# Kernel tuning notes

Measured on AMD Instinct MI355X. Metric: run time of the kernel, lower is better.

Reference implementation:

```python
import jax, jax.numpy as jnp
import numpy as np

B, L, DIM, HID, DSSH, DSSN = 2, 4096, 1024, 4096, 512, 512


def _ln(x, w, b):
    # LayerNorm over last dim, eps=1e-5 (torch default)
    m = x.mean(-1, keepdims=True)
    v = ((x - m) ** 2).mean(-1, keepdims=True)
    return (x - m) * jax.lax.rsqrt(v + 1e-5) * w + b


def _dss(x, n2_w, n2_b, LR, LI, CR, CI, D):
    # x: [B, L, dss_hidden]
    Lseq = x.shape[-2]
    xn = _ln(x, n2_w, n2_b)
    Lam = (-jnp.exp(LR) + 1j * jnp.exp(LI)).astype(jnp.complex64)        # [N]
    t = jnp.arange(Lseq, dtype=jnp.float32)
    S = jnp.exp(Lam[:, None] * t[None, :])                               # [N, L]
    Cc = (CR + 1j * CI) * ((jnp.exp(Lam) - 1.0) / Lam)                   # [H, N]
    K = jnp.einsum('hn,nl->lh', Cc, S).real                              # [L, H]
    n2 = 2 * Lseq
    Kf = jnp.fft.rfft(K, n=n2, axis=-2)                                  # [L+1, H]
    uf = jnp.fft.rfft(xn, n=n2, axis=-2)                                 # [B, L+1, H]
    y = jnp.fft.irfft(uf * Kf, n=n2, axis=-2)[..., :Lseq, :]
    return y + D * xn


def setup_inputs() -> dict:
    key = jax.random.key(0)
    ks = jax.random.split(key, 12)
    s = lambda k, sh, sc=1.0: jax.random.normal(k, sh, jnp.float32) * sc
    return dict(
        idx=s(ks[0], (B, L, DIM)),
        n1_w=jnp.ones((DIM,), jnp.float32), n1_b=jnp.zeros((DIM,), jnp.float32),
        Wxg=s(ks[1], (DIM, HID), 0.02),
        Wdin=s(ks[2], (DIM, DSSH), 0.02),
        n2_w=jnp.ones((DSSH,), jnp.float32), n2_b=jnp.zeros((DSSH,), jnp.float32),
        LR=s(ks[3], (DSSN,)), LI=s(ks[4], (DSSN,)),
        CR=s(ks[5], (DSSH, DSSN), 0.1), CI=s(ks[6], (DSSH, DSSN), 0.1),
        D=s(ks[7], (DSSH,)),
        Wgate=s(ks[8], (DSSH, HID), 0.02),
        Wout=s(ks[9], (HID, DIM), 0.02), bout=jnp.zeros((DIM,), jnp.float32),
    )


def reference(idx, n1_w, n1_b, Wxg, Wdin, n2_w, n2_b, LR, LI, CR, CI, D, Wgate, Wout, bout):
    x = _ln(idx, n1_w, n1_b)
    xg = x @ Wxg                                            # [B, L, HID]
    d = _dss(x @ Wdin, n2_w, n2_b, LR, LI, CR, CI, D)       # [B, L, DSSH]
    g = d @ Wgate                                           # [B, L, HID]
    out = (g * xg) @ Wout + bout                            # dropout is identity in eval
    return out + idx
```

## Files before the change

kernel.cpp:

```cpp
#include <hip/hip_runtime.h>
#include <math.h>


typedef unsigned short u16;
typedef unsigned int u32;
typedef __attribute__((ext_vector_type(8))) __bf16 bf16x8;
typedef __attribute__((ext_vector_type(4))) float f32x4;
typedef __attribute__((ext_vector_type(4))) u32 u32x4;

__device__ __forceinline__ u16 f2bf(float f) {
  u32 u = __float_as_uint(f);
  u32 r = u + 0x7FFFu + ((u >> 16) & 1u);
  return (u16)(r >> 16);
}
__device__ __forceinline__ float bf2f(u16 h) { return __uint_as_float(((u32)h) << 16); }

__global__ __launch_bounds__(256) void trans_conv(
    const float* __restrict__ in, u16* __restrict__ out, int K, int N) {
  __shared__ float t[32][33];
  int tx = threadIdx.x & 31, ty = threadIdx.x >> 5;
  int nb = N >> 5;
  int k0 = (blockIdx.x / nb) << 5;
  int n0 = (blockIdx.x % nb) << 5;
#pragma unroll
  for (int i = 0; i < 32; i += 8)
    t[ty + i][tx] = in[(size_t)(k0 + ty + i) * N + n0 + tx];
  __syncthreads();
#pragma unroll
  for (int i = 0; i < 32; i += 8)
    out[(size_t)(n0 + ty + i) * K + k0 + tx] = f2bf(t[tx][ty + i]);
}

__global__ __launch_bounds__(256) void trans_bf(
    const u16* __restrict__ in, u16* __restrict__ out, int R, int C) {
  __shared__ u16 t[32][34];
  int tx = threadIdx.x & 31, ty = threadIdx.x >> 5;
  int nb = C >> 5;
  int r0 = (blockIdx.x / nb) << 5;
  int c0 = (blockIdx.x % nb) << 5;
#pragma unroll
  for (int i = 0; i < 32; i += 8)
    t[ty + i][tx] = in[(size_t)(r0 + ty + i) * C + c0 + tx];
  __syncthreads();
#pragma unroll
  for (int i = 0; i < 32; i += 8)
    out[(size_t)(c0 + ty + i) * R + r0 + tx] = t[tx][ty + i];
}

template <bool BOUT>
__global__ void ln_kernel(const float* __restrict__ in, const float* __restrict__ gw,
                          const float* __restrict__ gb, void* outp, int D) {
  int row = blockIdx.x;
  int tid = threadIdx.x;
  const float4* r4 = (const float4*)(in + (size_t)row * D);
  float4 v = r4[tid];
  float s = v.x + v.y + v.z + v.w;
  float ss = fmaf(v.x, v.x, fmaf(v.y, v.y, fmaf(v.z, v.z, v.w * v.w)));
#pragma unroll
  for (int o = 32; o >= 1; o >>= 1) { s += __shfl_xor(s, o); ss += __shfl_xor(ss, o); }
  __shared__ float sa[8], sb[8];
  int nw = blockDim.x >> 6;
  if ((tid & 63) == 0) { sa[tid >> 6] = s; sb[tid >> 6] = ss; }
  __syncthreads();
  float S = 0.f, SS = 0.f;
  for (int i = 0; i < nw; ++i) { S += sa[i]; SS += sb[i]; }
  float mean = S / (float)D;
  float var = SS / (float)D - mean * mean;
  float inv = rsqrtf(var + 1e-5f);
  float4 wv = ((const float4*)gw)[tid];
  float4 bv = ((const float4*)gb)[tid];
  float o0 = (v.x - mean) * inv * wv.x + bv.x;
  float o1 = (v.y - mean) * inv * wv.y + bv.y;
  float o2 = (v.z - mean) * inv * wv.z + bv.z;
  float o3 = (v.w - mean) * inv * wv.w + bv.w;
  if (BOUT) {
    ushort4 o; o.x = f2bf(o0); o.y = f2bf(o1); o.z = f2bf(o2); o.w = f2bf(o3);
    ((ushort4*)outp)[(size_t)row * (D >> 2) + tid] = o;
  } else {
    float4 o; o.x = o0; o.y = o1; o.z = o2; o.w = o3;
    ((float4*)outp)[(size_t)row * (D >> 2) + tid] = o;
  }
}

__global__ __launch_bounds__(256) void ln_stats(
    const u16* __restrict__ xdTb, float* __restrict__ meanv, float* __restrict__ invv) {
  int lane = threadIdx.x & 63;
  int seg = threadIdx.x >> 6;
  int col = blockIdx.x * 64 + lane;
  float s = 0.f, ss = 0.f;
  const u16* p = xdTb + (size_t)(seg * 128) * 8192 + col;
#pragma unroll 8
  for (int r = 0; r < 128; ++r) {
    float v = bf2f(p[(size_t)r * 8192]);
    s += v; ss = fmaf(v, v, ss);
  }
  __shared__ float sa[4][64], sb[4][64];
  sa[seg][lane] = s; sb[seg][lane] = ss;
  __syncthreads();
  if (threadIdx.x < 64) {
    float S = sa[0][lane] + sa[1][lane] + sa[2][lane] + sa[3][lane];
    float SS = sb[0][lane] + sb[1][lane] + sb[2][lane] + sb[3][lane];
    float mean = S * (1.0f / 512.0f);
    float var = SS * (1.0f / 512.0f) - mean * mean;
    meanv[blockIdx.x * 64 + lane] = mean;
    invv[blockIdx.x * 64 + lane] = rsqrtf(var + 1e-5f);
  }
}

template <int MODE>
__global__ __launch_bounds__(256, 2) void gemm128p(
    const u16* __restrict__ A, const u16* __restrict__ Bt,
    int M, int N, int K,
    float* Cf, u16* Cb, const u16* aux,
    const float* __restrict__ bias, const float* __restrict__ res) {
  constexpr int BUF = 16384;
  __shared__ __align__(16) u16 lds[2 * BUF];
  const int tid = threadIdx.x;
  const int lane = tid & 63;
  const int w = tid >> 6;
  const int nwg = (int)gridDim.x;
  const int cpx = nwg >> 3;
  const int bid = (nwg & 7) ? (int)blockIdx.x
                            : ((int)blockIdx.x & 7) * cpx + ((int)blockIdx.x >> 3);
  const int tiles_n = N >> 7;
  const int tm = (bid / tiles_n) << 7;
  const int tn = (bid % tiles_n) << 7;

  const int wm = w >> 1, wn = w & 1;
  const int lr = lane & 15;
  const int kq = lane >> 4;
  const int l7 = lane & 7;
  const int rsub = lane >> 3;
  const int sslot = (lane & 7) ^ rsub;
  const u16* gA = A + (size_t)(tm + w * 32 + rsub) * K + sslot * 8;
  const u16* gB = Bt + (size_t)(tn + w * 32 + rsub) * K + sslot * 8;
  auto ldsc = (__attribute__((address_space(3))) char*)lds;

  auto STAGE = [&](int kt, int c) {
    const size_t kof = (size_t)kt << 6;
#pragma unroll
    for (int i = 0; i < 4; ++i) {
      u32 da = (u32)(c * BUF + (w * 32 + i * 8) * 64) * 2u;
      __builtin_amdgcn_global_load_lds(
          (const __attribute__((address_space(1))) void*)(gA + (size_t)(i * 8) * K + kof),
          (__attribute__((address_space(3))) void*)(ldsc + da), 16, 0, 0);
      __builtin_amdgcn_global_load_lds(
          (const __attribute__((address_space(1))) void*)(gB + (size_t)(i * 8) * K + kof),
          (__attribute__((address_space(3))) void*)(ldsc + da + 16384), 16, 0, 0);
    }
  };

  f32x4 acc[4][4] = {};
  const int NT = K >> 6;

  STAGE(0, 0);
  asm volatile("s_waitcnt vmcnt(0)" ::: "memory");
  __builtin_amdgcn_s_barrier();
  __builtin_amdgcn_sched_barrier(0);

  int cur = 0;
  for (int kt = 0; kt < NT; ++kt) {
    if (kt + 1 < NT) STAGE(kt + 1, cur ^ 1);
    const u32 ab = (u32)cur * BUF;
#pragma unroll
    for (int ks = 0; ks < 2; ++ks) {
      const int slp = ((((ks << 2) | kq)) ^ l7) << 3;
      bf16x8 af[4], bv[4];
#pragma unroll
      for (int mi = 0; mi < 4; ++mi) {
        int ra = wm * 64 + mi * 16 + lr;
        af[mi] = *(const bf16x8*)&lds[ab + ra * 64 + slp];
      }
#pragma unroll
      for (int ni = 0; ni < 4; ++ni) {
        int rb = wn * 64 + ni * 16 + lr;
        bv[ni] = *(const bf16x8*)&lds[ab + 8192 + rb * 64 + slp];
      }
      __builtin_amdgcn_s_setprio(1);
#pragma unroll
      for (int mi = 0; mi < 4; ++mi)
#pragma unroll
        for (int ni = 0; ni < 4; ++ni)
          acc[mi][ni] = __builtin_amdgcn_mfma_f32_16x16x32_bf16(af[mi], bv[ni], acc[mi][ni], 0, 0, 0);
      __builtin_amdgcn_s_setprio(0);
    }
    asm volatile("s_waitcnt vmcnt(0)" ::: "memory");
    __builtin_amdgcn_s_barrier();
    __builtin_amdgcn_sched_barrier(0);
    cur ^= 1;
  }

  float* lf = (float*)lds + w * (16 * 68);
  const int er = lane >> 2;
  const int ec = (lane & 3) << 4;
  const int gcol = tn + wn * 64 + ec;
#pragma unroll
  for (int mi = 0; mi < 4; ++mi) {
#pragma unroll
    for (int ni = 0; ni < 4; ++ni)
#pragma unroll
      for (int j = 0; j < 4; ++j)
        lf[(kq * 4 + j) * 68 + ni * 16 + lr] = acc[mi][ni][j];
    float v[16];
#pragma unroll
    for (int q = 0; q < 4; ++q)
      *(f32x4*)&v[q * 4] = *(const f32x4*)&lf[er * 68 + ec + q * 4];
    const int gr = tm + wm * 64 + mi * 16 + er;
    if (MODE == 3) {
      const float* rr = res + (size_t)gr * N + gcol;
      const float* br = bias + gcol;
      float* orr = Cf + (size_t)gr * N + gcol;
#pragma unroll
      for (int q = 0; q < 4; ++q) {
        f32x4 rv = *(const f32x4*)(rr + q * 4);
        f32x4 bv4 = *(const f32x4*)(br + q * 4);
        f32x4 ov;
        ov[0] = v[q * 4 + 0] + bv4[0] + rv[0];
        ov[1] = v[q * 4 + 1] + bv4[1] + rv[1];
        ov[2] = v[q * 4 + 2] + bv4[2] + rv[2];
        ov[3] = v[q * 4 + 3] + bv4[3] + rv[3];
        *(f32x4*)(orr + q * 4) = ov;
      }
    } else {
      u32 pk[8];
      if (MODE == 2) {
        const u16* ar = aux + (size_t)gr * N + gcol;
        u32x4 a0 = *(const u32x4*)ar;
        u32x4 a1 = *(const u32x4*)(ar + 8);
        u32 aw[8] = {a0[0], a0[1], a0[2], a0[3], a1[0], a1[1], a1[2], a1[3]};
#pragma unroll
        for (int e = 0; e < 8; ++e) {
          float m0 = v[2 * e] * bf2f((u16)(aw[e] & 0xffffu));
          float m1 = v[2 * e + 1] * bf2f((u16)(aw[e] >> 16));
          pk[e] = (u32)f2bf(m0) | ((u32)f2bf(m1) << 16);
        }
      } else {
#pragma unroll
        for (int e = 0; e < 8; ++e)
          pk[e] = (u32)f2bf(v[2 * e]) | ((u32)f2bf(v[2 * e + 1]) << 16);
      }
      u16* orr = Cb + (size_t)gr * N + gcol;
      *(u32x4*)orr = u32x4{pk[0], pk[1], pk[2], pk[3]};
      *(u32x4*)(orr + 8) = u32x4{pk[4], pk[5], pk[6], pk[7]};
    }
  }
}

__global__ __launch_bounds__(256) void kgen_s(
    const float* __restrict__ LR, const float* __restrict__ LI, u16* __restrict__ SRSI) {
  int idx0 = blockIdx.x * 256 + threadIdx.x;
  int l = idx0 >> 10;
  int kk = idx0 & 1023;
  int n = kk & 511;
  double a = exp((double)LR[n]);
  double om = exp((double)LI[n]);
  double ld = (double)l;
  float decay = (float)exp(-a * ld);
  double th = fmod(om * ld, 6.283185307179586477);
  float c, s;
  sincosf((float)th, &s, &c);
  SRSI[idx0] = f2bf(decay * ((kk < 512) ? c : s));
}

__global__ __launch_bounds__(256) void kgen_c(
    const float* __restrict__ LR, const float* __restrict__ LI,
    const float* __restrict__ CR, const float* __restrict__ CI, u16* __restrict__ Ct) {
  int idx0 = blockIdx.x * 256 + threadIdx.x;
  int h = idx0 >> 9, n = idx0 & 511;
  float eLR = expf(LR[n]), eLI = expf(LI[n]);
  float lre = -eLR, lim = eLI;
  float er = expf(lre);
  float c, s;
  sincosf(lim, &s, &c);
  float wr = er * c - 1.0f, wi = er * s;
  float den = lre * lre + lim * lim;
  float gr = (wr * lre + wi * lim) / den;
  float gi = (wi * lre - wr * lim) / den;
  float cr = CR[(size_t)h * 512 + n], ci = CI[(size_t)h * 512 + n];
  float ccr = cr * gr - ci * gi;
  float cci = cr * gi + ci * gr;
  Ct[(size_t)h * 1024 + n] = f2bf(ccr);
  Ct[(size_t)h * 1024 + 512 + n] = f2bf(-cci);
}

__global__ __launch_bounds__(256) void twfill(float4* __restrict__ twg4) {
  int j = blockIdx.x * 256 + threadIdx.x;
  float t1 = -6.2831853071795864769f * (float)j / 8192.0f;
  float s1, c1, s2, c2;
  sincosf(t1, &s1, &c1);
  sincosf(2.0f * t1, &s2, &c2);
  twg4[j] = {c1, s1, c2, s2};
}

struct C2 { float x, y; };
__device__ __forceinline__ C2 cadd(C2 a, C2 b) { return {a.x + b.x, a.y + b.y}; }
__device__ __forceinline__ C2 csub(C2 a, C2 b) { return {a.x - b.x, a.y - b.y}; }
__device__ __forceinline__ C2 cmul(C2 a, C2 b) {
  return {a.x * b.x - a.y * b.y, a.x * b.y + a.y * b.x};
}
__device__ __forceinline__ C2 cmulni(C2 a) { return {a.y, -a.x}; }

__device__ __forceinline__ int swz(int a) {
  return a ^ ((a >> 7) & 15) ^ ((a >> 11) & 3) ^ ((a >> 2) & 8) ^ ((a >> 3) & 2) ^ ((a >> 4) & 4);
}

#define BR13(x) ((int)(__brev((u32)(x)) >> 19))
#define RS 0.70710678118654752f

__device__ __forceinline__ void dif4(C2& a, C2& b, C2& c, C2& d, float4 wv) {
  C2 w = {wv.x, wv.y}, wm = {wv.y, -wv.x}, w2 = {wv.z, wv.w};
  C2 a1 = cadd(a, c);
  C2 c1 = cmul(csub(a, c), w);
  C2 b1 = cadd(b, d);
  C2 d1 = cmul(csub(b, d), wm);
  a = cadd(a1, b1);
  b = cmul(csub(a1, b1), w2);
  c = cadd(c1, d1);
  d = cmul(csub(c1, d1), w2);
}
__device__ __forceinline__ void dit4(C2& a, C2& b, C2& c, C2& d, float4 wv) {
  C2 w = {wv.x, wv.y}, wm = {wv.y, -wv.x}, wa = {wv.z, wv.w};
  C2 t = cmul(wa, b);
  C2 a1 = cadd(a, t), b1 = csub(a, t);
  C2 u = cmul(wa, d);
  C2 c1 = cadd(c, u), d1 = csub(c, u);
  C2 v = cmul(w, c1);
  C2 xx = cmul(wm, d1);
  a = cadd(a1, v);
  c = csub(a1, v);
  b = cadd(b1, xx);
  d = csub(b1, xx);
}

template <int L>
__device__ __forceinline__ void dif16(C2* z, int tid, const float4* __restrict__ twg4) {
  const int Q = 1 << (L - 2);
  const int pos2 = tid & (Q - 1);
  const int i0 = ((tid >> (L - 2)) << (L + 2)) | pos2;
  int ad[16]; C2 x[16];
#pragma unroll
  for (int k = 0; k < 16; ++k) { ad[k] = swz(i0 + k * Q); x[k] = z[ad[k]]; }
#pragma unroll
  for (int r = 0; r < 4; ++r)
    dif4(x[r], x[r + 4], x[r + 8], x[r + 12], twg4[(pos2 + r * Q) << (11 - L)]);
  {
    float4 wv2 = twg4[pos2 << (13 - L)];
#pragma unroll
    for (int m = 0; m < 4; ++m)
      dif4(x[4 * m], x[4 * m + 1], x[4 * m + 2], x[4 * m + 3], wv2);
  }
#pragma unroll
  for (int k = 0; k < 16; ++k) z[ad[k]] = x[k];
}
template <int L>
__device__ __forceinline__ void dit16(C2* z, int tid, const float4* __restrict__ twg4) {
  const int Q = 1 << (L - 2);
  const int pos2 = tid & (Q - 1);
  const int i0 = ((tid >> (L - 2)) << (L + 2)) | pos2;
  int ad[16]; C2 x[16];
#pragma unroll
  for (int k = 0; k < 16; ++k) { ad[k] = swz(i0 + k * Q); x[k] = z[ad[k]]; }
  {
    float4 wv2 = twg4[pos2 << (13 - L)];
#pragma unroll
    for (int m = 0; m < 4; ++m)
      dit4(x[4 * m], x[4 * m + 1], x[4 * m + 2], x[4 * m + 3], wv2);
  }
#pragma unroll
  for (int r = 0; r < 4; ++r)
    dit4(x[r], x[r + 4], x[r + 8], x[r + 12], twg4[(pos2 + r * Q) << (11 - L)]);
#pragma unroll
  for (int k = 0; k < 16; ++k) z[ad[k]] = x[k];
}

template <int LOGM>
__device__ __forceinline__ void dif_pass(C2* z, int tid, const float4* __restrict__ twg4) {
  const int M4 = 1 << LOGM;
#pragma unroll
  for (int j = 0; j < 4; ++j) {
    int b = tid + j * 512;
    int pos = b & (M4 - 1);
    int i0 = ((b >> LOGM) << (LOGM + 2)) | pos;
    int ia = swz(i0), ib = swz(i0 + M4), ic = swz(i0 + 2 * M4), id = swz(i0 + 3 * M4);
    C2 a = z[ia], bb = z[ib], c = z[ic], d = z[id];
    float4 wv = twg4[pos << (11 - LOGM)];
    dif4(a, bb, c, d, wv);
    z[ia] = a; z[ib] = bb; z[ic] = c; z[id] = d;
  }
}

template <int LOGM>
__device__ __forceinline__ void dit_pass(C2* z, int tid, const float4* __restrict__ twg4) {
  const int M4 = 1 << LOGM;
#pragma unroll
  for (int j = 0; j < 4; ++j) {
    int b = tid + j * 512;
    int pos = b & (M4 - 1);
    int i0 = ((b >> LOGM) << (LOGM + 2)) | pos;
    int ia = swz(i0), ib = swz(i0 + M4), ic = swz(i0 + 2 * M4), id = swz(i0 + 3 * M4);
    C2 a = z[ia], bb = z[ib], c = z[ic], d = z[id];
    float4 wv = twg4[pos << (11 - LOGM)];
    dit4(a, bb, c, d, wv);
    z[ia] = a; z[ib] = bb; z[ic] = c; z[id] = d;
  }
}

__device__ __forceinline__ void dif_r8(C2* z, int tid) {
#pragma unroll
  for (int j = 0; j < 2; ++j) {
    int base = (tid + j * 512) << 3;
    int ad[8]; C2 x[8];
#pragma unroll
    for (int e = 0; e < 8; ++e) { ad[e] = swz(base + e); x[e] = z[ad[e]]; }
    C2 t;
    t = csub(x[0], x[4]); x[0] = cadd(x[0], x[4]); x[4] = t;
    t = csub(x[1], x[5]); x[1] = cadd(x[1], x[5]); x[5] = cmul(t, {RS, -RS});
    t = csub(x[2], x[6]); x[2] = cadd(x[2], x[6]); x[6] = cmulni(t);
    t = csub(x[3], x[7]); x[3] = cadd(x[3], x[7]); x[7] = cmul(t, {-RS, -RS});
    t = csub(x[0], x[2]); x[0] = cadd(x[0], x[2]); x[2] = t;
    t = csub(x[1], x[3]); x[1] = cadd(x[1], x[3]); x[3] = cmulni(t);
    t = csub(x[4], x[6]); x[4] = cadd(x[4], x[6]); x[6] = t;
    t = csub(x[5], x[7]); x[5] = cadd(x[5], x[7]); x[7] = cmulni(t);
    t = csub(x[0], x[1]); x[0] = cadd(x[0], x[1]); x[1] = t;
    t = csub(x[2], x[3]); x[2] = cadd(x[2], x[3]); x[3] = t;
    t = csub(x[4], x[5]); x[4] = cadd(x[4], x[5]); x[5] = t;
    t = csub(x[6], x[7]); x[6] = cadd(x[6], x[7]); x[7] = t;
#pragma unroll
    for (int e = 0; e < 8; ++e) z[ad[e]] = x[e];
  }
}

__device__ __forceinline__ void r8_fused(C2* z, int tid, const u32* __restrict__ kfr) {
#pragma unroll
  for (int j = 0; j < 2; ++j) {
    int base = (tid + j * 512) << 3;
    int ad[8]; C2 x[8];
#pragma unroll
    for (int e = 0; e < 8; ++e) { ad[e] = swz(base + e); x[e] = z[ad[e]]; }
    u32x4 k0 = *(const u32x4*)(kfr + base);
    u32x4 k1 = *(const u32x4*)(kfr + base + 4);
    u32 kw[8] = {k0[0], k0[1], k0[2], k0[3], k1[0], k1[1], k1[2], k1[3]};
    C2 t;
    t = csub(x[0], x[4]); x[0] = cadd(x[0], x[4]); x[4] = t;
    t = csub(x[1], x[5]); x[1] = cadd(x[1], x[5]); x[5] = cmul(t, {RS, -RS});
    t = csub(x[2], x[6]); x[2] = cadd(x[2], x[6]); x[6] = cmulni(t);
    t = csub(x[3], x[7]); x[3] = cadd(x[3], x[7]); x[7] = cmul(t, {-RS, -RS});
    t = csub(x[0], x[2]); x[0] = cadd(x[0], x[2]); x[2] = t;
    t = csub(x[1], x[3]); x[1] = cadd(x[1], x[3]); x[3] = cmulni(t);
    t = csub(x[4], x[6]); x[4] = cadd(x[4], x[6]); x[6] = t;
    t = csub(x[5], x[7]); x[5] = cadd(x[5], x[7]); x[7] = cmulni(t);
    t = csub(x[0], x[1]); x[0] = cadd(x[0], x[1]); x[1] = t;
    t = csub(x[2], x[3]); x[2] = cadd(x[2], x[3]); x[3] = t;
    t = csub(x[4], x[5]); x[4] = cadd(x[4], x[5]); x[5] = t;
    t = csub(x[6], x[7]); x[6] = cadd(x[6], x[7]); x[7] = t;
#pragma unroll
    for (int e = 0; e < 8; ++e) {
      C2 kf = {bf2f((u16)(kw[e] & 0xffffu)), bf2f((u16)(kw[e] >> 16))};
      C2 pr = cmul(x[e], kf);
      x[e] = {pr.x, -pr.y};
    }
    t = x[1]; x[1] = csub(x[0], t); x[0] = cadd(x[0], t);
    t = x[3]; x[3] = csub(x[2], t); x[2] = cadd(x[2], t);
    t = x[5]; x[5] = csub(x[4], t); x[4] = cadd(x[4], t);
    t = x[7]; x[7] = csub(x[6], t); x[6] = cadd(x[6], t);
    t = x[2];          x[2] = csub(x[0], t); x[0] = cadd(x[0], t);
    t = cmulni(x[3]);  x[3] = csub(x[1], t); x[1] = cadd(x[1], t);
    t = x[6];          x[6] = csub(x[4], t); x[4] = cadd(x[4], t);
    t = cmulni(x[7]);  x[7] = csub(x[5], t); x[5] = cadd(x[5], t);
    t = x[4];                    x[4] = csub(x[0], t); x[0] = cadd(x[0], t);
    t = cmul(x[5], {RS, -RS});   x[5] = csub(x[1], t); x[1] = cadd(x[1], t);
    t = cmulni(x[6]);            x[6] = csub(x[2], t); x[2] = cadd(x[2], t);
    t = cmul(x[7], {-RS, -RS});  x[7] = csub(x[3], t); x[3] = cadd(x[3], t);
#pragma unroll
    for (int e = 0; e < 8; ++e) z[ad[e]] = x[e];
  }
}

__global__ __launch_bounds__(512) void kfft2(
    const u16* __restrict__ KTb, const float4* __restrict__ twg4,
    u32* __restrict__ Kfb) {
  __shared__ C2 z[8192];
  const int g = blockIdx.x;
  const int t = threadIdx.x;
  const u16* k0r = KTb + ((size_t)(2 * g) << 12);
  const u16* k1r = KTb + ((size_t)(2 * g + 1) << 12);

  C2 x[16];
#pragma unroll
  for (int k = 0; k < 8; ++k) {
    int l = t + k * 512;
    x[k] = {bf2f(k0r[l]), bf2f(k1r[l])};
  }
#pragma unroll
  for (int k = 8; k < 16; ++k) x[k] = {0.f, 0.f};
#pragma unroll
  for (int r = 0; r < 4; ++r)
    dif4(x[r], x[r + 4], x[r + 8], x[r + 12], twg4[t + r * 512]);
  {
    float4 wv2 = twg4[t << 2];
#pragma unroll
    for (int m = 0; m < 4; ++m)
      dif4(x[4 * m], x[4 * m + 1], x[4 * m + 2], x[4 * m + 3], wv2);
  }
#pragma unroll
  for (int k = 0; k < 16; ++k) z[swz(t + k * 512)] = x[k];
  __syncthreads();

  dif16<7>(z, t, twg4);   __syncthreads();
  dif_pass<3>(z, t, twg4); __syncthreads();
  dif_r8(z, t);            __syncthreads();

  u32* o0 = Kfb + ((size_t)(2 * g) << 13);
  u32* o1 = Kfb + ((size_t)(2 * g + 1) << 13);
#pragma unroll
  for (int it = 0; it < 16; ++it) {
    int p = t + it * 512;
    int k = BR13(p);
    int km = (8192 - k) & 8191;
    int p2 = BR13(km);
    C2 Zk = z[swz(p)], Zm = z[swz(p2)];
    float f0r = 0.5f * (Zk.x + Zm.x), f0i = 0.5f * (Zk.y - Zm.y);
    float f1r = 0.5f * (Zk.y + Zm.y), f1i = 0.5f * (Zm.x - Zk.x);
    o0[p] = (u32)f2bf(f0r) | ((u32)f2bf(f0i) << 16);
    o1[p] = (u32)f2bf(f1r) | ((u32)f2bf(f1i) << 16);
  }
}

__global__ __launch_bounds__(512) void fft_conv4(
    const u16* __restrict__ xdTb, const u32* __restrict__ Kfb,
    const float* __restrict__ meanv, const float* __restrict__ invv,
    const float* __restrict__ n2w, const float* __restrict__ n2b,
    const float* __restrict__ Dv, const float4* __restrict__ twg4,
    u16* __restrict__ dT) {
  __shared__ C2 z[8192];
  const int h = blockIdx.x;
  const int t = threadIdx.x;
  const u16* xr = xdTb + ((size_t)h << 13);
  const float w2h = n2w[h], b2h = n2b[h], Dh = Dv[h];

  float xn0r[8], xn1r[8];
  C2 x[16];
#pragma unroll
  for (int k = 0; k < 8; ++k) {
    int l = t + k * 512;
    float x0 = bf2f(xr[l]);
    float x1 = bf2f(xr[4096 + l]);
    xn0r[k] = (x0 - meanv[l]) * invv[l] * w2h + b2h;
    xn1r[k] = (x1 - meanv[4096 + l]) * invv[4096 + l] * w2h + b2h;
    x[k] = {xn0r[k], xn1r[k]};
  }
#pragma unroll
  for (int k = 8; k < 16; ++k) x[k] = {0.f, 0.f};
#pragma unroll
  for (int r = 0; r < 4; ++r)
    dif4(x[r], x[r + 4], x[r + 8], x[r + 12], twg4[t + r * 512]);
  {
    float4 wv2 = twg4[t << 2];
#pragma unroll
    for (int m = 0; m < 4; ++m)
      dif4(x[4 * m], x[4 * m + 1], x[4 * m + 2], x[4 * m + 3], wv2);
  }
#pragma unroll
  for (int k = 0; k < 16; ++k) z[swz(t + k * 512)] = x[k];
  __syncthreads();

  dif16<7>(z, t, twg4);    __syncthreads();
  dif_pass<3>(z, t, twg4);  __syncthreads();
  r8_fused(z, t, Kfb + ((size_t)h << 13)); __syncthreads();
  dit_pass<3>(z, t, twg4);  __syncthreads();
  dit16<7>(z, t, twg4);     __syncthreads();

#pragma unroll
  for (int k = 0; k < 16; ++k) x[k] = z[swz(t + k * 512)];
  {
    float4 wv2 = twg4[t << 2];
#pragma unroll
    for (int m = 0; m < 4; ++m)
      dit4(x[4 * m], x[4 * m + 1], x[4 * m + 2], x[4 * m + 3], wv2);
  }
  const float sc = 1.0f / 8192.0f;
  u16* drow = dT + ((size_t)h << 13);
#pragma unroll
  for (int r = 0; r < 4; ++r) {
    float4 wv = twg4[t + r * 512];
    C2 w = {wv.x, wv.y}, wm = {wv.y, -wv.x}, wa = {wv.z, wv.w};
    C2 a = x[r], bb = x[r + 4], c = x[r + 8], d = x[r + 12];
    C2 tt = cmul(wa, bb);
    C2 a1 = cadd(a, tt), b1 = csub(a, tt);
    C2 u = cmul(wa, d);
    C2 c1 = cadd(c, u), d1 = csub(c, u);
    C2 olo = cadd(a1, cmul(w, c1));
    C2 ohi = cadd(b1, cmul(wm, d1));
    int l0 = t + r * 512;
    int l1 = t + (r + 4) * 512;
    drow[l0] = f2bf(fmaf(Dh, xn0r[r], olo.x * sc));
    drow[4096 + l0] = f2bf(fmaf(Dh, xn1r[r], -olo.y * sc));
    drow[l1] = f2bf(fmaf(Dh, xn0r[r + 4], ohi.x * sc));
    drow[4096 + l1] = f2bf(fmaf(Dh, xn1r[r + 4], -ohi.y * sc));
  }
}

extern "C" void kernel_launch(void* const* d_in, const int* in_sizes, int n_in,
                              void* d_out, int out_size, void* d_ws, size_t ws_size,
                              hipStream_t stream) {
  (void)in_sizes; (void)n_in; (void)out_size; (void)ws_size;
  const float* idx  = (const float*)d_in[0];
  const float* n1w  = (const float*)d_in[1];
  const float* n1b  = (const float*)d_in[2];
  const float* Wxg  = (const float*)d_in[3];
  const float* Wdin = (const float*)d_in[4];
  const float* n2w  = (const float*)d_in[5];
  const float* n2b  = (const float*)d_in[6];
  const float* LR   = (const float*)d_in[7];
  const float* LI   = (const float*)d_in[8];
  const float* CR   = (const float*)d_in[9];
  const float* CI   = (const float*)d_in[10];
  const float* Dv   = (const float*)d_in[11];
  const float* Wgate= (const float*)d_in[12];
  const float* Wout = (const float*)d_in[13];
  const float* bout = (const float*)d_in[14];
  float* out = (float*)d_out;

  const int Bn = 2, L = 4096, DIM = 1024, HID = 4096, H = 512;
  const int M = Bn * L;

  char* p = (char*)d_ws;
  auto alloc = [&](size_t bytes) { char* q = p; p += (bytes + 255) & ~(size_t)255; return q; };
  u16* Wxg_t   = (u16*)alloc((size_t)HID * DIM * 2);
  u16* Wdin_t  = (u16*)alloc((size_t)H * DIM * 2);
  u16* Wgate_t = (u16*)alloc((size_t)HID * H * 2);
  u16* Wout_t  = (u16*)alloc((size_t)DIM * HID * 2);
  u16* xbf     = (u16*)alloc((size_t)M * DIM * 2);
  u16* xg      = (u16*)alloc((size_t)M * HID * 2);
  u16* xdTb    = (u16*)alloc((size_t)H * M * 2);
  float* meanv = (float*)alloc((size_t)M * 4);
  float* invv  = (float*)alloc((size_t)M * 4);
  u16* SRSI    = (u16*)alloc((size_t)L * 1024 * 2);
  u16* Ct      = (u16*)alloc((size_t)H * 1024 * 2);
  u16* KTb     = (u16*)alloc((size_t)H * L * 2);
  u16* dTm     = (u16*)alloc((size_t)H * M * 2);
  u16* dbuf    = (u16*)alloc((size_t)M * H * 2);
  float4* twg4 = (float4*)alloc((size_t)2048 * 16);
  u32* Kfb = (u32*)xbf;

  trans_conv<<<dim3((DIM / 32) * (HID / 32)), 256, 0, stream>>>(Wxg, Wxg_t, DIM, HID);
  trans_conv<<<dim3((DIM / 32) * (H / 32)), 256, 0, stream>>>(Wdin, Wdin_t, DIM, H);
  trans_conv<<<dim3((H / 32) * (HID / 32)), 256, 0, stream>>>(Wgate, Wgate_t, H, HID);
  trans_conv<<<dim3((HID / 32) * (DIM / 32)), 256, 0, stream>>>(Wout, Wout_t, HID, DIM);
  twfill<<<dim3(8), 256, 0, stream>>>(twg4);
  ln_kernel<true><<<dim3(M), 256, 0, stream>>>(idx, n1w, n1b, xbf, DIM);
  gemm128p<1><<<dim3((M / 128) * (HID / 128)), 256, 0, stream>>>(
      xbf, Wxg_t, M, HID, DIM, nullptr, xg, nullptr, nullptr, nullptr);
  gemm128p<1><<<dim3((H / 128) * (M / 128)), 256, 0, stream>>>(
      Wdin_t, xbf, H, M, DIM, nullptr, xdTb, nullptr, nullptr, nullptr);
  ln_stats<<<dim3(M / 64), 256, 0, stream>>>(xdTb, meanv, invv);
  kgen_s<<<dim3(L * 1024 / 256), 256, 0, stream>>>(LR, LI, SRSI);
  kgen_c<<<dim3(H * 512 / 256), 256, 0, stream>>>(LR, LI, CR, CI, Ct);
  gemm128p<1><<<dim3((H / 128) * (L / 128)), 256, 0, stream>>>(
      Ct, SRSI, H, L, 1024, nullptr, KTb, nullptr, nullptr, nullptr);
  kfft2<<<dim3(H / 2), 512, 0, stream>>>(KTb, twg4, Kfb);
  fft_conv4<<<dim3(H), 512, 0, stream>>>(xdTb, Kfb, meanv, invv, n2w, n2b, Dv, twg4, dTm);
  trans_bf<<<dim3((H / 32) * (M / 32)), 256, 0, stream>>>(dTm, dbuf, H, M);
  gemm128p<2><<<dim3((M / 128) * (HID / 128)), 256, 0, stream>>>(
      dbuf, Wgate_t, M, HID, H, nullptr, xg, xg, nullptr, nullptr);
  gemm128p<3><<<dim3((M / 128) * (DIM / 128)), 256, 0, stream>>>(
      xg, Wout_t, M, DIM, HID, out, nullptr, nullptr, bout, idx);
}
```

Baseline: 355.3 us.

## Fuse xg and gate GEMMs into one kernel with elementwise product epilogue

The x@Wxg GEMM and the d@Wgate GEMM are merged into one kernel. Each tile runs both K-loops back to back into two accumulator sets, multiplies them elementwise and writes the bf16 product once. This removes the bf16 round trip of the large xg intermediate (write, then re-read in the gate epilogue) and one launch. The cost is a second 64-register accumulator array, which may reduce occupancy or cause spills. Kfb now gets its own workspace allocation because xbf must stay live until the fused GEMM.

```diff
diff --git a/kernel.cpp b/kernel.cpp
--- a/kernel.cpp
+++ b/kernel.cpp
@@ -111,7 +111,7 @@
 __global__ __launch_bounds__(256, 2) void gemm128p(
     const u16* __restrict__ A, const u16* __restrict__ Bt,
     int M, int N, int K,
-    float* Cf, u16* Cb, const u16* aux,
+    float* Cf, u16* Cb,
     const float* __restrict__ bias, const float* __restrict__ res) {
   constexpr int BUF = 16384;
   __shared__ __align__(16) u16 lds[2 * BUF];
@@ -136,31 +136,31 @@
   const u16* gB = Bt + (size_t)(tn + w * 32 + rsub) * K + sslot * 8;
   auto ldsc = (__attribute__((address_space(3))) char*)lds;
 
-  auto STAGE = [&](int kt, int c) {
-    const size_t kof = (size_t)kt << 6;
-#pragma unroll
-    for (int i = 0; i < 4; ++i) {
-      u32 da = (u32)(c * BUF + (w * 32 + i * 8) * 64) * 2u;
-      __builtin_amdgcn_global_load_lds(
-          (const __attribute__((address_space(1))) void*)(gA + (size_t)(i * 8) * K + kof),
-          (__attribute__((address_space(3))) void*)(ldsc + da), 16, 0, 0);
-      __builtin_amdgcn_global_load_lds(
-          (const __attribute__((address_space(1))) void*)(gB + (size_t)(i * 8) * K + kof),
-          (__attribute__((address_space(3))) void*)(ldsc + da + 16384), 16, 0, 0);
-    }
-  };
+#define STAGE128(kt, c)                                                                   \
+  {                                                                                       \
+    const size_t kof = (size_t)(kt) << 6;                                                 \
+    _Pragma("unroll") for (int i = 0; i < 4; ++i) {                                       \
+      u32 da = (u32)((c)*BUF + (w * 32 + i * 8) * 64) * 2u;                               \
+      __builtin_amdgcn_global_load_lds(                                                   \
+          (const __attribute__((address_space(1))) void*)(gA + (size_t)(i * 8) * K + kof),\
+          (__attribute__((address_space(3))) void*)(ldsc + da), 16, 0, 0);                \
+      __builtin_amdgcn_global_load_lds(                                                   \
+          (const __attribute__((address_space(1))) void*)(gB + (size_t)(i * 8) * K + kof),\
+          (__attribute__((address_space(3))) void*)(ldsc + da + 16384), 16, 0, 0);        \
+    }                                                                                     \
+  }
 
   f32x4 acc[4][4] = {};
   const int NT = K >> 6;
 
-  STAGE(0, 0);
+  STAGE128(0, 0);
   asm volatile("s_waitcnt vmcnt(0)" ::: "memory");
   __builtin_amdgcn_s_barrier();
   __builtin_amdgcn_sched_barrier(0);
 
   int cur = 0;
   for (int kt = 0; kt < NT; ++kt) {
-    if (kt + 1 < NT) STAGE(kt + 1, cur ^ 1);
+    if (kt + 1 < NT) STAGE128(kt + 1, cur ^ 1);
     const u32 ab = (u32)cur * BUF;
 #pragma unroll
     for (int ks = 0; ks < 2; ++ks) {
@@ -189,6 +189,7 @@
     __builtin_amdgcn_sched_barrier(0);
     cur ^= 1;
   }
+#undef STAGE128
 
   float* lf = (float*)lds + w * (16 * 68);
   const int er = lane >> 2;
@@ -223,26 +224,137 @@
       }
     } else {
       u32 pk[8];
-      if (MODE == 2) {
-        const u16* ar = aux + (size_t)gr * N + gcol;
-        u32x4 a0 = *(const u32x4*)ar;
-        u32x4 a1 = *(const u32x4*)(ar + 8);
-        u32 aw[8] = {a0[0], a0[1], a0[2], a0[3], a1[0], a1[1], a1[2], a1[3]};
-#pragma unroll
-        for (int e = 0; e < 8; ++e) {
-          float m0 = v[2 * e] * bf2f((u16)(aw[e] & 0xffffu));
-          float m1 = v[2 * e + 1] * bf2f((u16)(aw[e] >> 16));
-          pk[e] = (u32)f2bf(m0) | ((u32)f2bf(m1) << 16);
-        }
-      } else {
-#pragma unroll
-        for (int e = 0; e < 8; ++e)
-          pk[e] = (u32)f2bf(v[2 * e]) | ((u32)f2bf(v[2 * e + 1]) << 16);
-      }
+#pragma unroll
+      for (int e = 0; e < 8; ++e)
+        pk[e] = (u32)f2bf(v[2 * e]) | ((u32)f2bf(v[2 * e + 1]) << 16);
       u16* orr = Cb + (size_t)gr * N + gcol;
       *(u32x4*)orr = u32x4{pk[0], pk[1], pk[2], pk[3]};
       *(u32x4*)(orr + 8) = u32x4{pk[4], pk[5], pk[6], pk[7]};
     }
+  }
+}
+
+__global__ __launch_bounds__(256, 2) void gemm_fuse2(
+    const u16* __restrict__ A1, const u16* __restrict__ B1t, int K1,
+    const u16* __restrict__ A2, const u16* __restrict__ B2t, int K2,
+    int M, int N, u16* __restrict__ Cb) {
+  constexpr int BUF = 16384;
+  __shared__ __align__(16) u16 lds[2 * BUF];
+  const int tid = threadIdx.x;
+  const int lane = tid & 63;
+  const int w = tid >> 6;
+  const int nwg = (int)gridDim.x;
+  const int cpx = nwg >> 3;
+  const int bid = (nwg & 7) ? (int)blockIdx.x
+                            : ((int)blockIdx.x & 7) * cpx + ((int)blockIdx.x >> 3);
+  const int tiles_n = N >> 7;
+  const int tm = (bid / tiles_n) << 7;
+  const int tn = (bid % tiles_n) << 7;
+
+  const int wm = w >> 1, wn = w & 1;
+  const int lr = lane & 15;
+  const int kq = lane >> 4;
+  const int l7 = lane & 7;
+  const int rsub = lane >> 3;
+  const int sslot = (lane & 7) ^ rsub;
+  auto ldsc = (__attribute__((address_space(3))) char*)lds;
+
+  f32x4 acc1[4][4] = {};
+  f32x4 acc2[4][4] = {};
+
+#define STAGEF(gA, gB, K, kt, c)                                                          \
+  {                                                                                       \
+    const size_t kof = (size_t)(kt) << 6;                                                 \
+    _Pragma("unroll") for (int i = 0; i < 4; ++i) {                                       \
+      u32 da = (u32)((c)*BUF + (w * 32 + i * 8) * 64) * 2u;                               \
+      __builtin_amdgcn_global_load_lds(                                                   \
+          (const __attribute__((address_space(1))) void*)((gA) + (size_t)(i * 8) * (K) + kof), \
+          (__attribute__((address_space(3))) void*)(ldsc + da), 16, 0, 0);                \
+      __builtin_amdgcn_global_load_lds(                                                   \
+          (const __attribute__((address_space(1))) void*)((gB) + (size_t)(i * 8) * (K) + kof), \
+          (__attribute__((address_space(3))) void*)(ldsc + da + 16384), 16, 0, 0);        \
+    }                                                                                     \
+  }
+
+#define KLOOP(gA, gB, K, ACC)                                                             \
+  {                                                                                       \
+    const int NT = (K) >> 6;                                                              \
+    STAGEF(gA, gB, K, 0, 0);                                                              \
+    asm volatile("s_waitcnt vmcnt(0)" ::: "memory");                                      \
+    __builtin_amdgcn_s_barrier();                                                         \
+    __builtin_amdgcn_sched_barrier(0);                                                    \
+    int cur = 0;                                                                          \
+    for (int kt = 0; kt < NT; ++kt) {                                                     \
+      if (kt + 1 < NT) STAGEF(gA, gB, K, kt + 1, cur ^ 1);                                \
+      const u32 ab = (u32)cur * BUF;                                                      \
+      _Pragma("unroll") for (int ks = 0; ks < 2; ++ks) {                                  \
+        const int slp = ((((ks << 2) | kq)) ^ l7) << 3;                                   \
+        bf16x8 af[4], bv[4];                                                              \
+        _Pragma("unroll") for (int mi = 0; mi < 4; ++mi) {                                \
+          int ra = wm * 64 + mi * 16 + lr;                                                \
+          af[mi] = *(const bf16x8*)&lds[ab + ra * 64 + slp];                              \
+        }                                                                                 \
+        _Pragma("unroll") for (int ni = 0; ni < 4; ++ni) {                                \
+          int rb = wn * 64 + ni * 16 + lr;                                                \
+          bv[ni] = *(const bf16x8*)&lds[ab + 8192 + rb * 64 + slp];                       \
+        }                                                                                 \
+        __builtin_amdgcn_s_setprio(1);                                                    \
+        _Pragma("unroll") for (int mi = 0; mi < 4; ++mi)                                  \
+          _Pragma("unroll") for (int ni = 0; ni < 4; ++ni)                                \
+            ACC[mi][ni] = __builtin_amdgcn_mfma_f32_16x16x32_bf16(af[mi], bv[ni], ACC[mi][ni], 0, 0, 0); \
+        __builtin_amdgcn_s_setprio(0);                                                    \
+      }                                                                                   \
+      asm volatile("s_waitcnt vmcnt(0)" ::: "memory");                                    \
+      __builtin_amdgcn_s_barrier();                                                       \
+      __builtin_amdgcn_sched_barrier(0);                                                  \
+      cur ^= 1;                                                                           \
+    }                                                                                     \
+  }
+
+  {
+    const u16* gA = A1 + (size_t)(tm + w * 32 + rsub) * K1 + sslot * 8;
+    const u16* gB = B1t + (size_t)(tn + w * 32 + rsub) * K1 + sslot * 8;
+    KLOOP(gA, gB, K1, acc1);
+  }
+  {
+    const u16* gA = A2 + (size_t)(tm + w * 32 + rsub) * K2 + sslot * 8;
+    const u16* gB = B2t + (size_t)(tn + w * 32 + rsub) * K2 + sslot * 8;
+    KLOOP(gA, gB, K2, acc2);
+  }
+#undef KLOOP
+#undef STAGEF
+
+#pragma unroll
+  for (int mi = 0; mi < 4; ++mi)
+#pragma unroll
+    for (int ni = 0; ni < 4; ++ni)
+#pragma unroll
+      for (int j = 0; j < 4; ++j)
+        acc1[mi][ni][j] *= acc2[mi][ni][j];
+
+  float* lf = (float*)lds + w * (16 * 68);
+  const int er = lane >> 2;
+  const int ec = (lane & 3) << 4;
+  const int gcol = tn + wn * 64 + ec;
+#pragma unroll
+  for (int mi = 0; mi < 4; ++mi) {
+#pragma unroll
+    for (int ni = 0; ni < 4; ++ni)
+#pragma unroll
+      for (int j = 0; j < 4; ++j)
+        lf[(kq * 4 + j) * 68 + ni * 16 + lr] = acc1[mi][ni][j];
+    float v[16];
+#pragma unroll
+    for (int q = 0; q < 4; ++q)
+      *(f32x4*)&v[q * 4] = *(const f32x4*)&lf[er * 68 + ec + q * 4];
+    const int gr = tm + wm * 64 + mi * 16 + er;
+    u32 pk[8];
+#pragma unroll
+    for (int e = 0; e < 8; ++e)
+      pk[e] = (u32)f2bf(v[2 * e]) | ((u32)f2bf(v[2 * e + 1]) << 16);
+    u16* orr = Cb + (size_t)gr * N + gcol;
+    *(u32x4*)orr = u32x4{pk[0], pk[1], pk[2], pk[3]};
+    *(u32x4*)(orr + 8) = u32x4{pk[4], pk[5], pk[6], pk[7]};
   }
 }
 
@@ -631,7 +743,7 @@
   u16* Wgate_t = (u16*)alloc((size_t)HID * H * 2);
   u16* Wout_t  = (u16*)alloc((size_t)DIM * HID * 2);
   u16* xbf     = (u16*)alloc((size_t)M * DIM * 2);
-  u16* xg      = (u16*)alloc((size_t)M * HID * 2);
+  u16* ebuf    = (u16*)alloc((size_t)M * HID * 2);
   u16* xdTb    = (u16*)alloc((size_t)H * M * 2);
   float* meanv = (float*)alloc((size_t)M * 4);
   float* invv  = (float*)alloc((size_t)M * 4);
@@ -641,7 +753,7 @@
   u16* dTm     = (u16*)alloc((size_t)H * M * 2);
   u16* dbuf    = (u16*)alloc((size_t)M * H * 2);
   float4* twg4 = (float4*)alloc((size_t)2048 * 16);
-  u32* Kfb = (u32*)xbf;
+  u32* Kfb     = (u32*)alloc((size_t)H * M * 4);
 
   trans_conv<<<dim3((DIM / 32) * (HID / 32)), 256, 0, stream>>>(Wxg, Wxg_t, DIM, HID);
   trans_conv<<<dim3((DIM / 32) * (H / 32)), 256, 0, stream>>>(Wdin, Wdin_t, DIM, H);
@@ -649,20 +761,18 @@
   trans_conv<<<dim3((HID / 32) * (DIM / 32)), 256, 0, stream>>>(Wout, Wout_t, HID, DIM);
   twfill<<<dim3(8), 256, 0, stream>>>(twg4);
   ln_kernel<true><<<dim3(M), 256, 0, stream>>>(idx, n1w, n1b, xbf, DIM);
-  gemm128p<1><<<dim3((M / 128) * (HID / 128)), 256, 0, stream>>>(
-      xbf, Wxg_t, M, HID, DIM, nullptr, xg, nullptr, nullptr, nullptr);
   gemm128p<1><<<dim3((H / 128) * (M / 128)), 256, 0, stream>>>(
-      Wdin_t, xbf, H, M, DIM, nullptr, xdTb, nullptr, nullptr, nullptr);
+      Wdin_t, xbf, H, M, DIM, nullptr, xdTb, nullptr, nullptr);
   ln_stats<<<dim3(M / 64), 256, 0, stream>>>(xdTb, meanv, invv);
   kgen_s<<<dim3(L * 1024 / 256), 256, 0, stream>>>(LR, LI, SRSI);
   kgen_c<<<dim3(H * 512 / 256), 256, 0, stream>>>(LR, LI, CR, CI, Ct);
   gemm128p<1><<<dim3((H / 128) * (L / 128)), 256, 0, stream>>>(
-      Ct, SRSI, H, L, 1024, nullptr, KTb, nullptr, nullptr, nullptr);
+      Ct, SRSI, H, L, 1024, nullptr, KTb, nullptr, nullptr);
   kfft2<<<dim3(H / 2), 512, 0, stream>>>(KTb, twg4, Kfb);
   fft_conv4<<<dim3(H), 512, 0, stream>>>(xdTb, Kfb, meanv, invv, n2w, n2b, Dv, twg4, dTm);
   trans_bf<<<dim3((H / 32) * (M / 32)), 256, 0, stream>>>(dTm, dbuf, H, M);
-  gemm128p<2><<<dim3((M / 128) * (HID / 128)), 256, 0, stream>>>(
-      dbuf, Wgate_t, M, HID, H, nullptr, xg, xg, nullptr, nullptr);
+  gemm_fuse2<<<dim3((M / 128) * (HID / 128)), 256, 0, stream>>>(
+      xbf, Wxg_t, DIM, dbuf, Wgate_t, H, M, HID, ebuf);
   gemm128p<3><<<dim3((M / 128) * (DIM / 128)), 256, 0, stream>>>(
-      xg, Wout_t, M, DIM, HID, out, nullptr, nullptr, bout, idx);
-}
+      ebuf, Wout_t, M, DIM, HID, out, nullptr, bout, idx);
+}
```

Result: faster. 344.1 us (-3.2%).
